# Performance work log

Hardware: AMD Instinct MI355X
Metric: run time of the kernel (lower is better)

## Reference

```python
import jax, jax.numpy as jnp
import numpy as np

B, S, E, H = 2, 2048, 1024, 16
D = E // H  # head_dim = 64


def setup_inputs() -> dict:
    key = jax.random.key(0)
    ks = jax.random.split(key, 6)
    scale = 1.0 / np.sqrt(E)
    x = jax.random.normal(ks[0], (B, S, E), dtype=jnp.float32)
    mask = jnp.ones((B, S), dtype=jnp.int32)
    Wqkv = jax.random.normal(ks[1], (E, 3 * E), dtype=jnp.float32) * scale
    bqkv = jax.random.normal(ks[2], (3 * E,), dtype=jnp.float32) * 0.01
    Wout = jax.random.normal(ks[3], (E, E), dtype=jnp.float32) * scale
    bout = jax.random.normal(ks[4], (E,), dtype=jnp.float32) * 0.01
    return {"x": x, "mask": mask, "Wqkv": Wqkv, "bqkv": bqkv, "Wout": Wout, "bout": bout}


def reference(x, mask, Wqkv, bqkv, Wout, bout):
    Bn, Sn, En = x.shape
    qkv = x @ Wqkv + bqkv                      # [B,S,3E]
    qkv = qkv.reshape(Bn, Sn, 3, H, D)
    qkv = jnp.transpose(qkv, (2, 0, 3, 1, 4))  # [3,B,H,S,D]
    q, k, v = qkv[0], qkv[1], qkv[2]
    scores = jnp.einsum('bhqd,bhkd->bhqk', q, k) / np.sqrt(D).astype(np.float32)
    m = mask[:, None, None, :]                 # [B,1,1,S]
    scores = jnp.where(m == 0, jnp.float32(-jnp.inf), scores)
    attn = jax.nn.softmax(scores, axis=-1)
    out = jnp.einsum('bhqk,bhkd->bhqd', attn, v)  # [B,H,S,D]
    out = jnp.transpose(out, (0, 2, 1, 3)).reshape(Bn, Sn, En)
    return out @ Wout + bout
```

## Files before the change

### kernel.cpp

```cpp
#include <hip/hip_runtime.h>


typedef __attribute__((ext_vector_type(8))) short short8;
typedef __attribute__((ext_vector_type(4))) short short4b;
typedef __attribute__((ext_vector_type(4))) float floatx4;
typedef __attribute__((ext_vector_type(16))) float floatx16;
typedef unsigned short ushort_t;

static __device__ __forceinline__ ushort_t f2bf(float f) {
    unsigned u = __float_as_uint(f);
    u += 0x7fffu + ((u >> 16) & 1u);
    return (ushort_t)(u >> 16);
}
static __device__ __forceinline__ float bf2f(ushort_t h) {
    return __uint_as_float(((unsigned)h) << 16);
}
#if __has_builtin(__builtin_amdgcn_cvt_pk_bf16_f32)
typedef __attribute__((ext_vector_type(2))) __bf16 bf16x2_t;
static __device__ __forceinline__ unsigned pack2bf(float a, float b) {
    bf16x2_t r = __builtin_amdgcn_cvt_pk_bf16_f32(a, b);
    return __builtin_bit_cast(unsigned, r);
}
#else
static __device__ __forceinline__ unsigned pack2bf(float a, float b) {
    return (unsigned)f2bf(a) | ((unsigned)f2bf(b) << 16);
}
#endif
static __device__ __forceinline__ float hexp2(float x) {
    return __builtin_amdgcn_exp2f(x);
}
static __device__ __forceinline__ void gload16(const void* g, void* l) {
    __builtin_amdgcn_global_load_lds(
        (const __attribute__((address_space(1))) unsigned int*)g,
        (__attribute__((address_space(3))) unsigned int*)l, 16, 0, 0);
}

#if __has_builtin(__builtin_amdgcn_permlane32_swap)
typedef __attribute__((ext_vector_type(2))) unsigned uint2v_t;
static __device__ __forceinline__ void plswap(unsigned x, unsigned y,
                                              unsigned& o0, unsigned& o1) {
    uint2v_t r = __builtin_amdgcn_permlane32_swap(x, y, false, false);
    o0 = r.x; o1 = r.y;
}
#else
static __device__ __forceinline__ void plswap(unsigned x, unsigned y,
                                              unsigned& o0, unsigned& o1) {
    int l = (int)(threadIdx.x & 63);
    bool hi = l >= 32;
    unsigned xsw = (unsigned)__shfl((int)x, l ^ 32);
    unsigned ysw = (unsigned)__shfl((int)y, l ^ 32);
    o0 = hi ? ysw : x;
    o1 = hi ? y : xsw;
}
#endif

__global__ __launch_bounds__(256) void prep(
    const float* __restrict__ x, ushort_t* __restrict__ xb,
    const float* __restrict__ Wqkv, ushort_t* __restrict__ wqT,
    const float* __restrict__ Wout, ushort_t* __restrict__ woT,
    const int* __restrict__ mask, float* __restrict__ maddg)
{
    __shared__ float tile[32][33];
    const int bk = blockIdx.x;
    const int t = threadIdx.x;
    if (bk < 4096) {
        int i = bk * 256 + t;
        float4 v = ((const float4*)x)[i];
        uint2 o;
        o.x = pack2bf(v.x, v.y);
        o.y = pack2bf(v.z, v.w);
        ((uint2*)xb)[i] = o;
        return;
    }
    if (bk < 8192) {
        const float* W; ushort_t* WT; int K, N, id;
        if (bk < 7168) { W = Wqkv; WT = wqT; K = 1024; N = 3072; id = bk - 4096;
                         int nb = (id % 96) * 32, kb = (id / 96) * 32;
                         const int r = t >> 3, c4 = (t & 7) * 4;
                         float4 v = *(const float4*)&W[(size_t)(kb + r) * N + nb + c4];
                         tile[r][c4+0]=v.x; tile[r][c4+1]=v.y; tile[r][c4+2]=v.z; tile[r][c4+3]=v.w;
                         __syncthreads();
                         uint2 o;
                         o.x = pack2bf(tile[c4+0][r], tile[c4+1][r]);
                         o.y = pack2bf(tile[c4+2][r], tile[c4+3][r]);
                         ((uint2*)WT)[((size_t)(nb + r) * K + kb + c4) >> 2] = o;
        } else {         W = Wout; WT = woT; K = 1024; N = 1024; id = bk - 7168;
                         int nb = (id % 32) * 32, kb = (id / 32) * 32;
                         const int r = t >> 3, c4 = (t & 7) * 4;
                         float4 v = *(const float4*)&W[(size_t)(kb + r) * N + nb + c4];
                         tile[r][c4+0]=v.x; tile[r][c4+1]=v.y; tile[r][c4+2]=v.z; tile[r][c4+3]=v.w;
                         __syncthreads();
                         uint2 o;
                         o.x = pack2bf(tile[c4+0][r], tile[c4+1][r]);
                         o.y = pack2bf(tile[c4+2][r], tile[c4+3][r]);
                         ((uint2*)WT)[((size_t)(nb + r) * K + kb + c4) >> 2] = o;
        }
        return;
    }
    {
        int i = (bk - 8192) * 256 + t;
        maddg[i] = (mask[i] ? 0.f : -1e30f) - 24.0f;
    }
}

__global__ __launch_bounds__(256, 3) void gemm_qkv(
    const ushort_t* __restrict__ A, const ushort_t* __restrict__ B,
    const float* __restrict__ bias, ushort_t* __restrict__ qkvb,
    ushort_t* __restrict__ vtg)
{
    const int K = 1024;
    __shared__ ushort_t Ah[128][32], Bh[128][32];
    __shared__ ushort_t Tb[64][136];
    const int bn = blockIdx.x * 128, bm = blockIdx.y * 128;
    const int t = threadIdx.x, w = t >> 6, lane = t & 63;
    const int l15 = lane & 15, quad = lane >> 4;
    const int wm = w >> 1, wn = w & 1;

    const int srow = w * 32 + (lane >> 2);
    const int skp  = (lane & 3) ^ ((lane >> 2) & 3);
    const int scol = skp * 8;
    const ushort_t* ga = A + (size_t)(bm + srow) * K + scol;
    const ushort_t* gb = B + (size_t)(bn + srow) * K + scol;
    const size_t rstep = (size_t)16 * K;
    const int fcol = ((quad ^ (l15 & 3)) * 8);

    floatx4 acc[4][4];
    #pragma unroll
    for (int mt = 0; mt < 4; ++mt)
        #pragma unroll
        for (int nt = 0; nt < 4; ++nt) acc[mt][nt] = (floatx4){0.f, 0.f, 0.f, 0.f};

    for (int k0 = 0; k0 < K; k0 += 32) {
        #pragma unroll
        for (int i = 0; i < 2; ++i) {
            gload16(ga + i * rstep + k0, &Ah[w * 32 + i * 16][0]);
            gload16(gb + i * rstep + k0, &Bh[w * 32 + i * 16][0]);
        }
        __syncthreads();
        short8 ah[4], bh[4];
        #pragma unroll
        for (int x = 0; x < 4; ++x) {
            ah[x] = *(const short8*)&Ah[wm * 64 + x * 16 + l15][fcol];
            bh[x] = *(const short8*)&Bh[wn * 64 + x * 16 + l15][fcol];
        }
        #pragma unroll
        for (int mt = 0; mt < 4; ++mt)
            #pragma unroll
            for (int nt = 0; nt < 4; ++nt)
                acc[mt][nt] = __builtin_amdgcn_mfma_f32_16x16x32_bf16(ah[mt], bh[nt], acc[mt][nt], 0, 0, 0);
        __syncthreads();
    }

    if (bn < 2048) {
        #pragma unroll
        for (int mt = 0; mt < 4; ++mt)
            #pragma unroll
            for (int r = 0; r < 4; ++r) {
                size_t row = (size_t)(bm + wm * 64 + mt * 16 + quad * 4 + r) * 2048;
                #pragma unroll
                for (int nt = 0; nt < 4; ++nt) {
                    int col = bn + wn * 64 + nt * 16 + l15;
                    qkvb[row + col] = f2bf(acc[mt][nt][r] + bias[col]);
                }
            }
    } else {
        const int h0 = (bn - 2048) >> 6;
        const int b  = bm >> 11, s0 = bm & 2047;
        #pragma unroll
        for (int hh = 0; hh < 2; ++hh) {
            if (wn == hh) {
                #pragma unroll
                for (int mt = 0; mt < 4; ++mt)
                    #pragma unroll
                    for (int nt = 0; nt < 4; ++nt) {
                        int d = nt * 16 + l15;
                        int sb = wm * 64 + mt * 16 + quad * 4;
                        float bv = bias[bn + hh * 64 + nt * 16 + l15];
                        uint2 pk;
                        pk.x = pack2bf(acc[mt][nt][0] + bv, acc[mt][nt][1] + bv);
                        pk.y = pack2bf(acc[mt][nt][2] + bv, acc[mt][nt][3] + bv);
                        *(uint2*)&Tb[d][sb] = pk;
                    }
            }
            __syncthreads();
            ushort_t* vbase = vtg + ((size_t)((b * 16 + h0 + hh) * 64)) * 2048 + s0;
            #pragma unroll
            for (int it = 0; it < 4; ++it) {
                int idx = t + it * 256;
                int d = idx >> 4, ch = idx & 15;
                uint4 v = *(const uint4*)&Tb[d][ch * 8];
                *(uint4*)&vbase[(size_t)d * 2048 + ch * 8] = v;
            }
            __syncthreads();
        }
    }
}

__global__ __launch_bounds__(256, 3) void gemm_bf16_f32_64(
    const ushort_t* __restrict__ A, const ushort_t* __restrict__ B,
    const float* __restrict__ bias, float* __restrict__ C,
    int M, int N, int K)
{
    __shared__ ushort_t Ah[64][32], Bh[128][32];
    const int bn = blockIdx.x * 128, bm = blockIdx.y * 64;
    const int t = threadIdx.x, w = t >> 6, lane = t & 63;
    const int l15 = lane & 15, quad = lane >> 4;
    const int wm = w >> 1, wn = w & 1;

    const int srow = w * 16 + (lane >> 2);
    const int skp  = (lane & 3) ^ ((lane >> 2) & 3);
    const int scol = skp * 8;
    const ushort_t* ga  = A + (size_t)(bm + srow) * K + scol;
    const ushort_t* gb0 = B + (size_t)(bn + srow) * K + scol;
    const ushort_t* gb1 = B + (size_t)(bn + 64 + srow) * K + scol;
    const int fcol = ((quad ^ (l15 & 3)) * 8);

    floatx4 acc[2][4];
    #pragma unroll
    for (int mt = 0; mt < 2; ++mt)
        #pragma unroll
        for (int nt = 0; nt < 4; ++nt) acc[mt][nt] = (floatx4){0.f, 0.f, 0.f, 0.f};

    for (int k0 = 0; k0 < K; k0 += 32) {
        gload16(ga  + k0, &Ah[w * 16][0]);
        gload16(gb0 + k0, &Bh[w * 16][0]);
        gload16(gb1 + k0, &Bh[64 + w * 16][0]);
        __syncthreads();
        short8 ah[2], bh[4];
        #pragma unroll
        for (int x = 0; x < 2; ++x)
            ah[x] = *(const short8*)&Ah[wm * 32 + x * 16 + l15][fcol];
        #pragma unroll
        for (int x = 0; x < 4; ++x)
            bh[x] = *(const short8*)&Bh[wn * 64 + x * 16 + l15][fcol];
        #pragma unroll
        for (int mt = 0; mt < 2; ++mt)
            #pragma unroll
            for (int nt = 0; nt < 4; ++nt)
                acc[mt][nt] = __builtin_amdgcn_mfma_f32_16x16x32_bf16(ah[mt], bh[nt], acc[mt][nt], 0, 0, 0);
        __syncthreads();
    }
    #pragma unroll
    for (int mt = 0; mt < 2; ++mt)
        #pragma unroll
        for (int r = 0; r < 4; ++r) {
            size_t row = (size_t)(bm + wm * 32 + mt * 16 + quad * 4 + r) * N;
            #pragma unroll
            for (int nt = 0; nt < 4; ++nt) {
                int col = bn + wn * 64 + nt * 16 + l15;
                C[row + col] = acc[mt][nt][r] + bias[col];
            }
        }
}

__global__ __launch_bounds__(256, 2) void flash_v10(
    const ushort_t* __restrict__ qkv, const ushort_t* __restrict__ vtg,
    const float* __restrict__ maddg, ushort_t* __restrict__ attn)
{
    __shared__ ushort_t Ks[2][64][64];
    __shared__ ushort_t Vt[2][64][64];

    const int blk = blockIdx.x;
    const int xcd = blk & 7, rr = blk >> 3;
    const int qi = rr & 15, g = xcd + 8 * (rr >> 4);
    const int b = g >> 4, h = g & 15, q0 = qi * 128;

    const int t = threadIdx.x, wave = t >> 6, lane = t & 63;
    const int l31 = lane & 31, hi = lane >> 5, l7 = lane & 7;
    const size_t bS = (size_t)b * 2048;
    const float c1 = 0.125f * 1.44269504088896340736f;

    short8 qf[4];
    {
        int q = q0 + wave * 32 + l31;
        const ushort_t* qp = qkv + (bS + q) * 2048 + h * 64 + hi * 8;
        #pragma unroll
        for (int ks = 0; ks < 4; ++ks)
            qf[ks] = *(const short8*)(qp + ks * 16);
    }

    const int srow  = wave * 16 + (lane >> 3);
    const int schnk = ((lane & 7) ^ ((lane >> 3) & 7)) * 8;
    const ushort_t* gK = qkv + (bS + srow) * 2048 + 1024 + h * 64 + schnk;
    const ushort_t* gV = vtg + ((size_t)(b * 16 + h) * 64 + srow) * 2048 + schnk;
    const float* gM = maddg + b * 2048;

    gload16(gK,            &Ks[0][wave * 16][0]);
    gload16(gK + 8 * 2048, &Ks[0][wave * 16 + 8][0]);
    gload16(gV,            &Vt[0][wave * 16][0]);
    gload16(gV + 8 * 2048, &Vt[0][wave * 16 + 8][0]);
    __syncthreads();

    floatx16 outacc[2] = {};
    float lsum = 0.f;

    int cur = 0;
    for (int kt = 0; kt < 32; ++kt) {
        const int k0 = kt * 64;
        {
            const int kn = (kt + 1 < 32) ? (kt + 1) * 64 : 0;
            const int nb = cur ^ 1;
            gload16(gK + (size_t)kn * 2048,       &Ks[nb][wave * 16][0]);
            gload16(gK + (size_t)(kn + 8) * 2048, &Ks[nb][wave * 16 + 8][0]);
            gload16(gV + kn,                      &Vt[nb][wave * 16][0]);
            gload16(gV + kn + 8 * 2048,           &Vt[nb][wave * 16 + 8][0]);
        }
        float4 m4[2][4];
        #pragma unroll
        for (int t32 = 0; t32 < 2; ++t32)
            #pragma unroll
            for (int gr = 0; gr < 4; ++gr)
                m4[t32][gr] = *(const float4*)&gM[k0 + t32 * 32 + gr * 8 + hi * 4];

        floatx16 sc[2] = {};
        __builtin_amdgcn_s_setprio(1);
        #pragma unroll
        for (int t32 = 0; t32 < 2; ++t32)
            #pragma unroll
            for (int ks = 0; ks < 4; ++ks) {
                const int ch = ((2 * ks + hi) ^ l7) * 8;
                short8 ka = *(const short8*)&Ks[cur][t32 * 32 + l31][ch];
                sc[t32] = __builtin_amdgcn_mfma_f32_32x32x16_bf16(ka, qf[ks], sc[t32], 0, 0, 0);
            }
        __builtin_amdgcn_s_setprio(0);

        unsigned W[2][4][2];
        #pragma unroll
        for (int t32 = 0; t32 < 2; ++t32)
            #pragma unroll
            for (int gr = 0; gr < 4; ++gr) {
                float p0 = hexp2(fmaf(sc[t32][gr * 4 + 0], c1, m4[t32][gr].x));
                float p1 = hexp2(fmaf(sc[t32][gr * 4 + 1], c1, m4[t32][gr].y));
                float p2 = hexp2(fmaf(sc[t32][gr * 4 + 2], c1, m4[t32][gr].z));
                float p3 = hexp2(fmaf(sc[t32][gr * 4 + 3], c1, m4[t32][gr].w));
                lsum += (p0 + p1) + (p2 + p3);
                W[t32][gr][0] = pack2bf(p0, p1);
                W[t32][gr][1] = pack2bf(p2, p3);
            }

        #pragma unroll
        for (int ks2 = 0; ks2 < 4; ++ks2) {
            const int t32 = ks2 >> 1;
            const int ae  = (ks2 & 1) * 2;
            uint4 u;
            plswap(W[t32][ae][0], W[t32][ae + 1][0], u.x, u.z);
            plswap(W[t32][ae][1], W[t32][ae + 1][1], u.y, u.w);
            short8 pb = __builtin_bit_cast(short8, u);
            const int ch = ((2 * ks2 + hi) ^ l7) * 8;
            __builtin_amdgcn_s_setprio(1);
            #pragma unroll
            for (int dt = 0; dt < 2; ++dt) {
                short8 va = *(const short8*)&Vt[cur][dt * 32 + l31][ch];
                outacc[dt] = __builtin_amdgcn_mfma_f32_32x32x16_bf16(va, pb, outacc[dt], 0, 0, 0);
            }
            __builtin_amdgcn_s_setprio(0);
        }
        __syncthreads();
        cur ^= 1;
    }

    {
        lsum += __shfl_xor(lsum, 32);
        float inv = 1.f / lsum;
        int q = q0 + wave * 32 + l31;
        ushort_t* orow = attn + (bS + q) * 1024 + h * 64;
        #pragma unroll
        for (int dt = 0; dt < 2; ++dt)
            #pragma unroll
            for (int gr = 0; gr < 4; ++gr) {
                uint2 pk;
                pk.x = pack2bf(outacc[dt][gr * 4 + 0] * inv, outacc[dt][gr * 4 + 1] * inv);
                pk.y = pack2bf(outacc[dt][gr * 4 + 2] * inv, outacc[dt][gr * 4 + 3] * inv);
                *(uint2*)&orow[dt * 32 + gr * 8 + hi * 4] = pk;
            }
    }
}

extern "C" void kernel_launch(void* const* d_in, const int* in_sizes, int n_in,
                              void* d_out, int out_size, void* d_ws, size_t ws_size,
                              hipStream_t stream) {
    const float* x    = (const float*)d_in[0];
    const int*   mask = (const int*)  d_in[1];
    const float* Wqkv = (const float*)d_in[2];
    const float* bqkv = (const float*)d_in[3];
    const float* Wout = (const float*)d_in[4];
    const float* bout = (const float*)d_in[5];
    float* out = (float*)d_out;

    char* ws = (char*)d_ws;
    ushort_t* xb    = (ushort_t*)(ws);
    ushort_t* wqT   = (ushort_t*)(ws + 8388608);
    ushort_t* qkvb  = (ushort_t*)(ws + 14680064);
    ushort_t* vtg   = (ushort_t*)(ws + 31457280);
    ushort_t* attnb = (ushort_t*)(ws + 39845888);
    ushort_t* woT   = (ushort_t*)(ws + 48234496);
    float*    maddg = (float*)   (ws + 50331648);

    const int M = 4096, E = 1024, N3 = 3072;

    prep<<<dim3(8208), dim3(256), 0, stream>>>(
        x, xb, Wqkv, wqT, Wout, woT, mask, maddg);

    gemm_qkv<<<dim3(N3 / 128, M / 128), dim3(256), 0, stream>>>(
        xb, wqT, bqkv, qkvb, vtg);

    flash_v10<<<dim3(512), dim3(256), 0, stream>>>(qkvb, vtg, maddg, attnb);

    gemm_bf16_f32_64<<<dim3(E / 128, M / 64), dim3(256), 0, stream>>>(
        attnb, woT, bout, out, M, E, E);
}
```

Measured before the change: 203.0 us.

## Split attention key range across two wave groups per block and merge partials

The flash attention kernel now launches 512 threads per block, with two halves of four waves each processing half of the key sequence (1024 keys) for the same 128 queries. At the end, the second half writes its output accumulators and row sums to shared memory, and the first half adds them and normalises. This doubles the active waves per query tile and halves the serial key-loop length, so more latency can be hidden on a grid of only 512 blocks. In exchange it doubles LDS use and adds a reduction step through shared memory. Merging without a max rescale is safe here because the original kernel already uses an unnormalised exp with no running max.

```diff
diff --git a/kernel.cpp b/kernel.cpp
--- a/kernel.cpp
+++ b/kernel.cpp
@@ -253,12 +253,12 @@
         }
 }
 
-__global__ __launch_bounds__(256, 2) void flash_v10(
+__global__ __launch_bounds__(512, 4) void flash_v11(
     const ushort_t* __restrict__ qkv, const ushort_t* __restrict__ vtg,
     const float* __restrict__ maddg, ushort_t* __restrict__ attn)
 {
-    __shared__ ushort_t Ks[2][64][64];
-    __shared__ ushort_t Vt[2][64][64];
+    __shared__ __align__(16) ushort_t Ks[2][2][64][64];
+    __shared__ __align__(16) ushort_t Vt[2][2][64][64];
 
     const int blk = blockIdx.x;
     const int xcd = blk & 7, rr = blk >> 3;
@@ -266,44 +266,45 @@
     const int b = g >> 4, h = g & 15, q0 = qi * 128;
 
     const int t = threadIdx.x, wave = t >> 6, lane = t & 63;
+    const int half = wave >> 2, wsub = wave & 3;
     const int l31 = lane & 31, hi = lane >> 5, l7 = lane & 7;
     const size_t bS = (size_t)b * 2048;
     const float c1 = 0.125f * 1.44269504088896340736f;
 
     short8 qf[4];
     {
-        int q = q0 + wave * 32 + l31;
+        int q = q0 + wsub * 32 + l31;
         const ushort_t* qp = qkv + (bS + q) * 2048 + h * 64 + hi * 8;
         #pragma unroll
         for (int ks = 0; ks < 4; ++ks)
             qf[ks] = *(const short8*)(qp + ks * 16);
     }
 
-    const int srow  = wave * 16 + (lane >> 3);
+    const int srow  = wsub * 16 + (lane >> 3);
     const int schnk = ((lane & 7) ^ ((lane >> 3) & 7)) * 8;
-    const ushort_t* gK = qkv + (bS + srow) * 2048 + 1024 + h * 64 + schnk;
-    const ushort_t* gV = vtg + ((size_t)(b * 16 + h) * 64 + srow) * 2048 + schnk;
-    const float* gM = maddg + b * 2048;
-
-    gload16(gK,            &Ks[0][wave * 16][0]);
-    gload16(gK + 8 * 2048, &Ks[0][wave * 16 + 8][0]);
-    gload16(gV,            &Vt[0][wave * 16][0]);
-    gload16(gV + 8 * 2048, &Vt[0][wave * 16 + 8][0]);
+    const ushort_t* gK = qkv + (bS + half * 1024 + srow) * 2048 + 1024 + h * 64 + schnk;
+    const ushort_t* gV = vtg + ((size_t)(b * 16 + h) * 64 + srow) * 2048 + half * 1024 + schnk;
+    const float* gM = maddg + b * 2048 + half * 1024;
+
+    gload16(gK,            &Ks[half][0][wsub * 16][0]);
+    gload16(gK + 8 * 2048, &Ks[half][0][wsub * 16 + 8][0]);
+    gload16(gV,            &Vt[half][0][wsub * 16][0]);
+    gload16(gV + 8 * 2048, &Vt[half][0][wsub * 16 + 8][0]);
     __syncthreads();
 
     floatx16 outacc[2] = {};
     float lsum = 0.f;
 
     int cur = 0;
-    for (int kt = 0; kt < 32; ++kt) {
+    for (int kt = 0; kt < 16; ++kt) {
         const int k0 = kt * 64;
-        {
-            const int kn = (kt + 1 < 32) ? (kt + 1) * 64 : 0;
+        if (kt + 1 < 16) {
+            const int kn = (kt + 1) * 64;
             const int nb = cur ^ 1;
-            gload16(gK + (size_t)kn * 2048,       &Ks[nb][wave * 16][0]);
-            gload16(gK + (size_t)(kn + 8) * 2048, &Ks[nb][wave * 16 + 8][0]);
-            gload16(gV + kn,                      &Vt[nb][wave * 16][0]);
-            gload16(gV + kn + 8 * 2048,           &Vt[nb][wave * 16 + 8][0]);
+            gload16(gK + (size_t)kn * 2048,       &Ks[half][nb][wsub * 16][0]);
+            gload16(gK + (size_t)(kn + 8) * 2048, &Ks[half][nb][wsub * 16 + 8][0]);
+            gload16(gV + kn,                      &Vt[half][nb][wsub * 16][0]);
+            gload16(gV + kn + 8 * 2048,           &Vt[half][nb][wsub * 16 + 8][0]);
         }
         float4 m4[2][4];
         #pragma unroll
@@ -319,7 +320,7 @@
             #pragma unroll
             for (int ks = 0; ks < 4; ++ks) {
                 const int ch = ((2 * ks + hi) ^ l7) * 8;
-                short8 ka = *(const short8*)&Ks[cur][t32 * 32 + l31][ch];
+                short8 ka = *(const short8*)&Ks[half][cur][t32 * 32 + l31][ch];
                 sc[t32] = __builtin_amdgcn_mfma_f32_32x32x16_bf16(ka, qf[ks], sc[t32], 0, 0, 0);
             }
         __builtin_amdgcn_s_setprio(0);
@@ -350,7 +351,7 @@
             __builtin_amdgcn_s_setprio(1);
             #pragma unroll
             for (int dt = 0; dt < 2; ++dt) {
-                short8 va = *(const short8*)&Vt[cur][dt * 32 + l31][ch];
+                short8 va = *(const short8*)&Vt[half][cur][dt * 32 + l31][ch];
                 outacc[dt] = __builtin_amdgcn_mfma_f32_32x32x16_bf16(va, pb, outacc[dt], 0, 0, 0);
             }
             __builtin_amdgcn_s_setprio(0);
@@ -359,20 +360,38 @@
         cur ^= 1;
     }
 
-    {
-        lsum += __shfl_xor(lsum, 32);
-        float inv = 1.f / lsum;
-        int q = q0 + wave * 32 + l31;
+    lsum += __shfl_xor(lsum, 32);
+
+    float* Obuf = (float*)&Ks[0][0][0][0];
+    float* Lbuf = (float*)&Vt[0][0][0][0];
+
+    if (half == 1) {
+        #pragma unroll
+        for (int dt = 0; dt < 2; ++dt)
+            #pragma unroll
+            for (int i = 0; i < 16; ++i)
+                Obuf[(wsub * 64 + lane) * 32 + ((dt * 16 + i) ^ l31)] = outacc[dt][i];
+        Lbuf[wsub * 32 + l31] = lsum;
+    }
+    __syncthreads();
+    if (half == 0) {
+        float inv = 1.f / (lsum + Lbuf[wsub * 32 + l31]);
+        int q = q0 + wsub * 32 + l31;
         ushort_t* orow = attn + (bS + q) * 1024 + h * 64;
         #pragma unroll
-        for (int dt = 0; dt < 2; ++dt)
+        for (int dt = 0; dt < 2; ++dt) {
+            float o[16];
+            #pragma unroll
+            for (int i = 0; i < 16; ++i)
+                o[i] = outacc[dt][i] + Obuf[(wsub * 64 + lane) * 32 + ((dt * 16 + i) ^ l31)];
             #pragma unroll
             for (int gr = 0; gr < 4; ++gr) {
                 uint2 pk;
-                pk.x = pack2bf(outacc[dt][gr * 4 + 0] * inv, outacc[dt][gr * 4 + 1] * inv);
-                pk.y = pack2bf(outacc[dt][gr * 4 + 2] * inv, outacc[dt][gr * 4 + 3] * inv);
+                pk.x = pack2bf(o[gr * 4 + 0] * inv, o[gr * 4 + 1] * inv);
+                pk.y = pack2bf(o[gr * 4 + 2] * inv, o[gr * 4 + 3] * inv);
                 *(uint2*)&orow[dt * 32 + gr * 8 + hi * 4] = pk;
             }
+        }
     }
 }
 
@@ -404,7 +423,7 @@
     gemm_qkv<<<dim3(N3 / 128, M / 128), dim3(256), 0, stream>>>(
         xb, wqT, bqkv, qkvb, vtg);
 
-    flash_v10<<<dim3(512), dim3(256), 0, stream>>>(qkvb, vtg, maddg, attnb);
+    flash_v11<<<dim3(512), dim3(512), 0, stream>>>(qkvb, vtg, maddg, attnb);
 
     gemm_bf16_f32_64<<<dim3(E / 128, M / 64), dim3(256), 0, stream>>>(
         attnb, woT, bout, out, M, E, E);
```

Measured after the change: 212.5 us. 4.7% more time.
